# Optimization experiments

Hardware: AMD Instinct MI355X
Metric: run time of the kernel (lower is better)

Reference implementation:

```python
import jax, jax.numpy as jnp
import numpy as np
from jax import lax

NPOINT = 1024
NSAMPLE = 64
RADIUS = 0.2
EPS = 1e-5  # BatchNorm eps


def farthest_point_sample(xyz, npoint):
    # xyz: [B, N, 3] -> idx [B, npoint]; deterministic init at point 0
    B, N, _ = xyz.shape

    def step(carry, _):
        dist, farthest = carry
        centroid = jnp.take_along_axis(xyz, farthest[:, None, None], axis=1)  # [B,1,3]
        d = jnp.sum((xyz - centroid) ** 2, axis=-1)  # [B,N]
        dist = jnp.minimum(dist, d)
        new_far = jnp.argmax(dist, axis=-1).astype(jnp.int32)
        return (dist, new_far), farthest

    init = (jnp.full((B, N), 1e10, xyz.dtype), jnp.zeros((B,), jnp.int32))
    _, idxs = lax.scan(step, init, None, length=npoint)
    return jnp.transpose(idxs)  # [B, npoint]


def square_distance(src, dst):
    # src [B,S,3], dst [B,N,3] -> [B,S,N]
    d = -2.0 * jnp.einsum('bsc,bnc->bsn', src, dst)
    d += jnp.sum(src ** 2, -1)[:, :, None]
    d += jnp.sum(dst ** 2, -1)[:, None, :]
    return d


def query_ball_point(radius, nsample, xyz, new_xyz):
    B, N, _ = xyz.shape
    sqr = square_distance(new_xyz, xyz)  # [B,S,N]
    gi = jnp.where(sqr > radius ** 2, N, jnp.arange(N, dtype=jnp.int32))
    gi = jnp.sort(gi, axis=-1)[:, :, :nsample]  # [B,S,K]
    first = gi[:, :, :1]
    gi = jnp.where(gi == N, first, gi)
    return gi


def mlp_bn_relu(x, W, g, b):
    # x [B,S,K,Cin], W [Cin,Cout]; 1x1 conv + training-mode BN + ReLU
    y = jnp.einsum('bskc,co->bsko', x, W)
    m = jnp.mean(y, axis=(0, 1, 2))
    v = jnp.var(y, axis=(0, 1, 2))
    y = (y - m) * lax.rsqrt(v + EPS) * g + b
    return jax.nn.relu(y)


def setup_inputs() -> dict:
    key = jax.random.key(0)
    ks = jax.random.split(key, 8)
    B, N, C = 8, 4096, 128
    xyz = jax.random.uniform(ks[0], (B, N, 3), dtype=jnp.float32)
    features = jax.random.normal(ks[1], (B, C, N), dtype=jnp.float32)
    c_in = C + 3  # use_xyz
    W1 = jax.random.normal(ks[2], (c_in, 128), dtype=jnp.float32) * 0.05
    W2 = jax.random.normal(ks[3], (128, 128), dtype=jnp.float32) * 0.05
    W3 = jax.random.normal(ks[4], (128, 256), dtype=jnp.float32) * 0.05
    return {
        'xyz': xyz, 'features': features,
        'W1': W1, 'g1': jnp.ones((128,)), 'b1': jnp.zeros((128,)),
        'W2': W2, 'g2': jnp.ones((128,)), 'b2': jnp.zeros((128,)),
        'W3': W3, 'g3': jnp.ones((256,)), 'b3': jnp.zeros((256,)),
    }


def reference(xyz, features, W1, g1, b1, W2, g2, b2, W3, g3, b3):
    fps_idx = farthest_point_sample(xyz, NPOINT)              # [B,S]
    new_xyz = jnp.take_along_axis(xyz, fps_idx[:, :, None], axis=1)  # [B,S,3]
    gi = query_ball_point(RADIUS, NSAMPLE, xyz, new_xyz)      # [B,S,K]
    gather = jax.vmap(lambda p, i: p[i])                      # per-batch gather
    grouped_xyz = gather(xyz, gi) - new_xyz[:, :, None, :]    # [B,S,K,3]
    grouped_feat = gather(jnp.transpose(features, (0, 2, 1)), gi)  # [B,S,K,C]
    x = jnp.concatenate([grouped_xyz, grouped_feat], axis=-1)  # [B,S,K,3+C]
    x = mlp_bn_relu(x, W1, g1, b1)
    x = mlp_bn_relu(x, W2, g2, b2)
    x = mlp_bn_relu(x, W3, g3, b3)
    new_features = jnp.transpose(jnp.max(x, axis=2), (0, 2, 1))  # [B,256,S]
    return new_xyz, new_features
```

## Files before the change

kernel.cpp:

```cpp
#include <hip/hip_runtime.h>

#define B_  8
#define N_  4096
#define S_  1024
#define K_  64
#define CF_ 128
#define M_  (B_*S_*K_)

typedef __attribute__((ext_vector_type(8))) short bshort8;
typedef __attribute__((ext_vector_type(4))) float f32x4;
typedef __attribute__((ext_vector_type(4))) int   i32x4;
typedef __attribute__((ext_vector_type(2))) float f32x2;
typedef __attribute__((ext_vector_type(4))) unsigned short us4;

__device__ __forceinline__ unsigned short f2bf(float f){
  unsigned int u = __float_as_uint(f);
  u = u + 0x7FFFu + ((u >> 16) & 1u);
  return (unsigned short)(u >> 16);
}
__device__ __forceinline__ float bf2f(unsigned short h){
  return __uint_as_float(((unsigned int)h) << 16);
}

__device__ __forceinline__ void fused_stats(float* __restrict__ slots,
                                            const float* __restrict__ g,
                                            const float* __restrict__ beta,
                                            float* __restrict__ ssOut,
                                            int C, int* __restrict__ ctr,
                                            int nblocks, int t){
  __shared__ int lastFlag;
  __syncthreads();
  if (t == 0) lastFlag = (atomicAdd(ctr, 1) == nblocks - 1);
  __syncthreads();
  if (!lastFlag) return;
  if (t < C){
    const float inv_cnt = 1.0f/524288.0f;
    float s = 0.f, s2 = 0.f;
    for (int k = 0; k < 64; ++k){
      s  += atomicAdd(&slots[(k*C + t)*2 + 0], 0.0f);
      s2 += atomicAdd(&slots[(k*C + t)*2 + 1], 0.0f);
    }
    float m  = s * inv_cnt;
    float v  = fmaxf(s2 * inv_cnt - m*m, 0.f);
    float sc = rsqrtf(v + 1e-5f) * g[t];
    ssOut[t]     = sc;
    ssOut[C + t] = beta[t] - m*sc;
  }
}

__global__ __launch_bounds__(256) void prep_kernel(const float* __restrict__ f,
                                                   const float* __restrict__ W1,
                                                   const float* __restrict__ W2,
                                                   const float* __restrict__ W3,
                                                   unsigned short* __restrict__ ft,
                                                   unsigned short* __restrict__ Wt1,
                                                   unsigned short* __restrict__ Wt2,
                                                   unsigned short* __restrict__ Wt3){
  __shared__ float tile[32][33];
  const int blk = blockIdx.x;
  if (blk < 4096){
    int nt = blk & 127, ct = (blk>>7)&3, b = blk>>9;
    int tx = threadIdx.x & 31, ty = threadIdx.x >> 5;
#pragma unroll
    for (int r=0; r<32; r+=8)
      tile[ty+r][tx] = f[((size_t)(b*128 + ct*32 + ty + r))*4096 + nt*32 + tx];
    __syncthreads();
#pragma unroll
    for (int r=0; r<32; r+=8){
      int n = nt*32 + ty + r, cc = ct*32 + tx;
      ft[((size_t)b*4096 + n)*128 + cc] = f2bf(tile[tx][ty+r]);
    }
  } else {
    int t = (blk-4096)*256 + threadIdx.x;
    int stride = 64*256;
    for (int idx=t; idx<128*160; idx+=stride){
      int n = idx/160, k = idx-(idx/160)*160;
      float v = 0.f;
      if (k < 128) v = W1[(k+3)*128 + n];
      else if (k < 131) v = W1[(k-128)*128 + n];
      Wt1[idx] = f2bf(v);
    }
    for (int idx=t; idx<128*128; idx+=stride){
      int n = idx>>7, k = idx&127;
      Wt2[idx] = f2bf(W2[k*128+n]);
    }
    for (int idx=t; idx<256*128; idx+=stride){
      int n = idx>>7, k = idx&127;
      Wt3[idx] = f2bf(W3[k*256+n]);
    }
  }
}

__global__ __launch_bounds__(256,2) void pgemm_kernel(const unsigned short* __restrict__ featT,
                                                      const unsigned short* __restrict__ Wt1,
                                                      float* __restrict__ P){
  __shared__ alignas(16) unsigned short At[128*40];
  __shared__ alignas(16) unsigned short Bt[128*40];
  const int t = threadIdx.x, blk = blockIdx.x;
  const size_t rowBase = (size_t)blk*128;
  const int lane = t&63, wave = t>>6;
  const int wm = wave>>1, wn = wave&1;
  const int lrow = lane&15, quad = lane>>4;
  f32x4 acc[4][4];
  const f32x4 z4 = {0.f,0.f,0.f,0.f};
#pragma unroll
  for (int i=0;i<4;++i)
#pragma unroll
    for (int j=0;j<4;++j) acc[i][j]=z4;
  for (int ch=0; ch<4; ++ch){
    __syncthreads();
#pragma unroll
    for (int half=0; half<2; ++half){
      int sl = t + half*256; int r = sl>>2, p = sl&3;
      *(bshort8*)&At[r*40+p*8] = *(const bshort8*)(featT + (rowBase + r)*CF_ + ch*32 + p*8);
      *(bshort8*)&Bt[r*40+p*8] = *(const bshort8*)(Wt1 + r*160 + ch*32 + p*8);
    }
    __syncthreads();
    bshort8 af[4], bfr[4];
#pragma unroll
    for (int mt=0; mt<4; ++mt) af[mt]  = *(const bshort8*)&At[(wm*64+mt*16+lrow)*40 + quad*8];
#pragma unroll
    for (int nt=0; nt<4; ++nt) bfr[nt] = *(const bshort8*)&Bt[(wn*64+nt*16+lrow)*40 + quad*8];
#pragma unroll
    for (int mt=0; mt<4; ++mt)
#pragma unroll
      for (int nt=0; nt<4; ++nt)
        acc[mt][nt] = __builtin_amdgcn_mfma_f32_16x16x32_bf16(af[mt], bfr[nt], acc[mt][nt], 0,0,0);
  }
#pragma unroll
  for (int mt=0; mt<4; ++mt)
#pragma unroll
    for (int nt=0; nt<4; ++nt)
#pragma unroll
      for (int r=0; r<4; ++r){
        int row = wm*64 + mt*16 + quad*4 + r;
        int col = wn*64 + nt*16 + lrow;
        P[(rowBase + row)*128 + col] = acc[mt][nt][r];
      }
}

#define DPP_PAIR_STEP(CTRL)                                                     \
  {                                                                             \
    int _vi = __builtin_amdgcn_update_dpp(__float_as_int(best), __float_as_int(best), (CTRL), 0xF, 0xF, false); \
    int _ii = __builtin_amdgcn_update_dpp(bidx, bidx, (CTRL), 0xF, 0xF, false); \
    float _ov = __int_as_float(_vi);                                            \
    bool _tk = (_ov > best) || (_ov == best && _ii < bidx);                     \
    best = _tk ? _ov : best;                                                    \
    bidx = _tk ? _ii : bidx;                                                    \
  }

__global__ __launch_bounds__(256) void fps_kernel(const float* __restrict__ xyz,
                                                  float* __restrict__ nx_out,
                                                  float* __restrict__ nx_ws){
#pragma clang fp contract(off)
  __shared__ float sx[N_], sy[N_], sz[N_];
  __shared__ int   sidx[S_];
  __shared__ alignas(16) float redv[2][4];
  __shared__ alignas(16) int   redi[2][4];
  const int b = blockIdx.x, t = threadIdx.x;
  const int lane = t & 63, w = t >> 6;
  const float* xb = xyz + (size_t)b*N_*3;
  f32x2 px[8], py[8], pz[8], dist[8];
#pragma unroll
  for (int j=0;j<8;++j){
    int i0 = (2*j)*256 + t, i1 = (2*j+1)*256 + t;
    float x0=xb[i0*3+0], y0=xb[i0*3+1], z0=xb[i0*3+2];
    float x1=xb[i1*3+0], y1=xb[i1*3+1], z1=xb[i1*3+2];
    px[j] = (f32x2){x0,x1}; py[j] = (f32x2){y0,y1}; pz[j] = (f32x2){z0,z1};
    dist[j] = (f32x2){1e10f,1e10f};
    sx[i0]=x0; sy[i0]=y0; sz[i0]=z0;
    sx[i1]=x1; sy[i1]=y1; sz[i1]=z1;
  }
  __syncthreads();
  int farthest = 0;
  for (int it=0; it<S_; ++it){
    if (t==0) sidx[it] = farthest;
    float cx = sx[farthest], cy = sy[farthest], cz = sz[farthest];
    f32x2 cx2 = (f32x2){cx,cx}, cy2 = (f32x2){cy,cy}, cz2 = (f32x2){cz,cz};
    float best = -1.0f; int bidx = 0;
#pragma unroll
    for (int j=0;j<8;++j){
      f32x2 dx = px[j] - cx2;
      f32x2 dy = py[j] - cy2;
      f32x2 dz = pz[j] - cz2;
      f32x2 d  = (dx*dx + dy*dy) + dz*dz;
      f32x2 nd;
      nd.x = fminf(dist[j].x, d.x);
      nd.y = fminf(dist[j].y, d.y);
      dist[j] = nd;
      bool tk0 = nd.x > best;
      best = tk0 ? nd.x : best;
      bidx = tk0 ? ((2*j)*256 + t) : bidx;
      bool tk1 = nd.y > best;
      best = tk1 ? nd.y : best;
      bidx = tk1 ? ((2*j+1)*256 + t) : bidx;
    }
    DPP_PAIR_STEP(0xB1);
    DPP_PAIR_STEP(0x4E);
    DPP_PAIR_STEP(0x124);
    DPP_PAIR_STEP(0x128);
    DPP_PAIR_STEP(0x142);
    DPP_PAIR_STEP(0x143);
    const int buf = it & 1;
    if (lane == 63){ redv[buf][w] = best; redi[buf][w] = bidx; }
    __syncthreads();
    f32x4 vv = *(const f32x4*)&redv[buf][0];
    i32x4 iv = *(const i32x4*)&redi[buf][0];
    float v01 = vv[0]; int i01 = iv[0];
    { bool tk = (vv[1] > v01) || (vv[1] == v01 && iv[1] < i01); v01 = tk?vv[1]:v01; i01 = tk?iv[1]:i01; }
    float v23 = vv[2]; int i23 = iv[2];
    { bool tk = (vv[3] > v23) || (vv[3] == v23 && iv[3] < i23); v23 = tk?vv[3]:v23; i23 = tk?iv[3]:i23; }
    { bool tk = (v23 > v01) || (v23 == v01 && i23 < i01); v01 = tk?v23:v01; i01 = tk?i23:i01; }
    farthest = i01;
  }
  __syncthreads();
  for (int i=t; i<S_; i+=256){
    int id = sidx[i];
    size_t base = (size_t)(b*S_+i)*3;
    float vx=sx[id], vy=sy[id], vz=sz[id];
    nx_out[base+0]=vx; nx_out[base+1]=vy; nx_out[base+2]=vz;
    nx_ws[base+0]=vx;  nx_ws[base+1]=vy;  nx_ws[base+2]=vz;
  }
}

__global__ __launch_bounds__(256) void qbp_y1_kernel(const float* __restrict__ xyz,
                                                     const float* __restrict__ nx,
                                                     const float* __restrict__ P,
                                                     const float* __restrict__ W1,
                                                     int* __restrict__ gi,
                                                     float* __restrict__ slots,
                                                     const float* __restrict__ g1,
                                                     const float* __restrict__ b1,
                                                     float* __restrict__ ss1,
                                                     int* __restrict__ ctr){
  __shared__ int giW[4][64];
  __shared__ alignas(16) float dxL[4][64][4];
  __shared__ float sLDS[128], s2LDS[128];
  const int t = threadIdx.x;
  const int lane = t & 63, w = t >> 6;
  if (t < 128){ sLDS[t]=0.f; s2LDS[t]=0.f; }
  __syncthreads();
  const int wid = blockIdx.x*4 + w;
  const int b = wid >> 10, s = wid & 1023;
  const float* xb = xyz + (size_t)b*N_*3;
  {
    const double R2 = 0.2*0.2;
    const float* c  = nx + (size_t)(b*S_+s)*3;
    double cx=(double)c[0], cy=(double)c[1], cz=(double)c[2];
    double cc = cx*cx + cy*cy + cz*cz;
    int* g = gi + (size_t)(b*S_+s)*K_;
    int count = 0, first = -1;
    for (int ch=0; ch<64 && count<K_; ++ch){
      int i = ch*64 + lane;
      double x = (double)xb[i*3+0], y = (double)xb[i*3+1], z = (double)xb[i*3+2];
      double e  = cx*x + cy*y + cz*z;
      double pp = x*x + y*y + z*z;
      double d  = -2.0*e + cc + pp;
      bool keep = !(d > R2);
      unsigned long long bal = __ballot(keep);
      int pos = count + __builtin_popcountll(bal & ((1ull<<lane)-1ull));
      if (keep && pos < K_){ g[pos] = i; giW[w][pos] = i; }
      if (first < 0 && bal) first = ch*64 + (int)__builtin_ctzll(bal);
      count += __builtin_popcountll(bal);
    }
    if (count < K_){
      int p = count + lane;
      if (p < K_){ g[p] = first; giW[w][p] = first; }
    }
    int i = giW[w][lane];
    const float* pp = xyz + ((size_t)b*N_ + i)*3;
    const float* qq = nx  + (size_t)(b*S_ + s)*3;
    dxL[w][lane][0] = __fsub_rn(pp[0],qq[0]);
    dxL[w][lane][1] = __fsub_rn(pp[1],qq[1]);
    dxL[w][lane][2] = __fsub_rn(pp[2],qq[2]);
  }
  {
    const int cq = lane*2;
    f32x2 w0 = *(const f32x2*)(W1 + cq);
    f32x2 w1v = *(const f32x2*)(W1 + 128 + cq);
    f32x2 w2 = *(const f32x2*)(W1 + 256 + cq);
    f32x2 sA = {0,0}, s2A = {0,0};
#pragma unroll 4
    for (int r=0; r<64; ++r){
      int pi = giW[w][r];
      f32x2 p = *(const f32x2*)(P + ((size_t)b*N_ + pi)*128 + cq);
      float dx = dxL[w][r][0], dy = dxL[w][r][1], dz = dxL[w][r][2];
      f32x2 y;
#pragma unroll
      for (int e=0;e<2;++e)
        y[e] = fmaf(dz, w2[e], fmaf(dy, w1v[e], fmaf(dx, w0[e], p[e])));
      sA.x += y.x; sA.y += y.y;
      s2A.x = fmaf(y.x,y.x,s2A.x); s2A.y = fmaf(y.y,y.y,s2A.y);
    }
    atomicAdd(&sLDS[cq],    sA.x);  atomicAdd(&sLDS[cq+1],  sA.y);
    atomicAdd(&s2LDS[cq],   s2A.x); atomicAdd(&s2LDS[cq+1], s2A.y);
  }
  __syncthreads();
  if (t < 128){
    int slot = blockIdx.x & 63;
    atomicAdd(&slots[(slot*128+t)*2+0], sLDS[t]);
    atomicAdd(&slots[(slot*128+t)*2+1], s2LDS[t]);
  }
  fused_stats(slots, g1, b1, ss1, 128, ctr, 2048, t);
}

template<int PHASE, bool STOREY2>
__global__ __launch_bounds__(256,2) void mm_fused(
    const float* __restrict__ P,
    const float* __restrict__ W1,
    const unsigned short* __restrict__ Wt2,
    const unsigned short* __restrict__ Wt3,
    const int* __restrict__ gi,
    const float* __restrict__ xyz,
    const float* __restrict__ nxyz,
    const float* __restrict__ ss1,
    const float* __restrict__ ss2,
    float* __restrict__ slots,
    float* __restrict__ minv,
    float* __restrict__ maxv,
    unsigned short* __restrict__ y2out,
    const float* __restrict__ gg,
    const float* __restrict__ bb,
    float* __restrict__ ssOut,
    int* __restrict__ ctr)
{
  __shared__ alignas(16) unsigned short Bt[2][128*40];
  __shared__ alignas(16) unsigned short Y[128*136];
  __shared__ int giL[128];
  __shared__ alignas(16) float dxL[128][4];
  __shared__ alignas(16) float w0L[128], w1L[128], w2L[128];

  const int t = threadIdx.x;
  const int mblk = blockIdx.x;
  const int b = mblk >> 9;
  const int lane = t&63, wave = t>>6;
  const int wm = wave>>1, wn = wave&1;
  const int lrow = lane&15, quad = lane>>4;
  const int slot = mblk & 63;

  if (t<128){
    int i = gi[(size_t)mblk*128 + t];
    giL[t] = i;
    int s = ((mblk*128 + t) >> 6) & 1023;
    const float* pp = xyz  + ((size_t)b*N_ + i)*3;
    const float* qq = nxyz + (size_t)(b*S_ + s)*3;
    dxL[t][0] = __fsub_rn(pp[0],qq[0]);
    dxL[t][1] = __fsub_rn(pp[1],qq[1]);
    dxL[t][2] = __fsub_rn(pp[2],qq[2]);
    w0L[t] = W1[t]; w1L[t] = W1[128+t]; w2L[t] = W1[256+t];
  }
  __syncthreads();

  {
    const int rgrp = t>>5, cq = (t&31)*4;
    f32x4 w0 = *(const f32x4*)&w0L[cq];
    f32x4 w1 = *(const f32x4*)&w1L[cq];
    f32x4 w2 = *(const f32x4*)&w2L[cq];
    f32x4 a1v = *(const f32x4*)(ss1 + cq);
    f32x4 b1v = *(const f32x4*)(ss1 + 128 + cq);
#pragma unroll
    for (int g=0; g<16; ++g){
      int r = g*8 + rgrp;
      int pi = giL[r];
      f32x4 p = *(const f32x4*)(P + ((size_t)b*N_ + pi)*128 + cq);
      float dx = dxL[r][0], dy = dxL[r][1], dz = dxL[r][2];
      f32x4 y;
#pragma unroll
      for (int e=0;e<4;++e)
        y[e] = fmaf(dz, w2[e], fmaf(dy, w1[e], fmaf(dx, w0[e], p[e])));
      us4 zz;
#pragma unroll
      for (int e=0;e<4;++e)
        zz[e] = f2bf(fmaxf(fmaf(y[e], a1v[e], b1v[e]), 0.f));
      *(us4*)&Y[r*136 + cq] = zz;
    }
  }

  f32x4 acc[4][4];
  const f32x4 z4 = {0.f,0.f,0.f,0.f};
#pragma unroll
  for (int i=0;i<4;++i)
#pragma unroll
    for (int j=0;j<4;++j) acc[i][j]=z4;

  {
    bshort8 bV[2];
#pragma unroll
    for (int half=0; half<2; ++half){
      int sl = t + half*256; int r = sl>>2, p = sl&3;
      bV[half] = *(const bshort8*)(Wt2 + r*128 + p*8);
    }
#pragma unroll
    for (int half=0; half<2; ++half){
      int sl = t + half*256; int r = sl>>2, p = sl&3;
      *(bshort8*)&Bt[1][r*40+p*8] = bV[half];
    }
    for (int ch=0; ch<4; ++ch){
      const int cur = (ch & 1) ^ 1;
      __syncthreads();
      bshort8 af[4], bfr[4];
#pragma unroll
      for (int mt=0; mt<4; ++mt) af[mt]  = *(const bshort8*)&Y[(wm*64+mt*16+lrow)*136 + ch*32 + quad*8];
#pragma unroll
      for (int nt=0; nt<4; ++nt) bfr[nt] = *(const bshort8*)&Bt[cur][(wn*64+nt*16+lrow)*40 + quad*8];
      if (ch < 3){
#pragma unroll
        for (int half=0; half<2; ++half){
          int sl = t + half*256; int r = sl>>2, p = sl&3;
          bV[half] = *(const bshort8*)(Wt2 + r*128 + (ch+1)*32 + p*8);
        }
      }
#pragma unroll
      for (int mt=0; mt<4; ++mt)
#pragma unroll
        for (int nt=0; nt<4; ++nt)
          acc[mt][nt] = __builtin_amdgcn_mfma_f32_16x16x32_bf16(af[mt], bfr[nt], acc[mt][nt], 0,0,0);
      if (ch < 3){
        const int nxt = cur ^ 1;
#pragma unroll
        for (int half=0; half<2; ++half){
          int sl = t + half*256; int r = sl>>2, p = sl&3;
          *(bshort8*)&Bt[nxt][r*40+p*8] = bV[half];
        }
      }
    }
  }

  if constexpr (PHASE==2){
#pragma unroll
    for (int nt=0; nt<4; ++nt){
      float s=0.f, s2=0.f;
#pragma unroll
      for (int mt=0; mt<4; ++mt)
#pragma unroll
        for (int r=0; r<4; ++r){ float v=acc[mt][nt][r]; s+=v; s2=fmaf(v,v,s2); }
      s  += __shfl_xor(s,16,64);  s  += __shfl_xor(s,32,64);
      s2 += __shfl_xor(s2,16,64); s2 += __shfl_xor(s2,32,64);
      if (lane<16){
        int c = wn*64+nt*16+lane;
        atomicAdd(&slots[(slot*128+c)*2+0], s);
        atomicAdd(&slots[(slot*128+c)*2+1], s2);
      }
    }
    if constexpr (STOREY2){
      __syncthreads();
#pragma unroll
      for (int nt=0; nt<4; ++nt){
        int c = wn*64+nt*16+lrow;
#pragma unroll
        for (int mt=0; mt<4; ++mt)
#pragma unroll
          for (int r=0; r<4; ++r){
            int row = wm*64+mt*16+quad*4+r;
            Y[row*136 + c] = f2bf(acc[mt][nt][r]);
          }
      }
      __syncthreads();
      for (int idx=t; idx<128*16; idx+=256){
        int r = idx>>4, p = idx&15;
        bshort8 v = *(const bshort8*)&Y[r*136 + p*8];
        *(bshort8*)(y2out + ((size_t)mblk*128 + r)*128 + p*8) = v;
      }
    }
    fused_stats(slots, gg, bb, ssOut, 128, ctr, 4096, t);
    return;
  }

  if constexpr (PHASE==3){
    __syncthreads();
#pragma unroll
    for (int nt=0; nt<4; ++nt){
      int c = wn*64+nt*16+lrow;
      float sc = ss2[c], sh = ss2[128+c];
#pragma unroll
      for (int mt=0; mt<4; ++mt)
#pragma unroll
        for (int r=0; r<4; ++r){
          int row = wm*64+mt*16+quad*4+r;
          Y[row*136 + c] = f2bf(fmaxf(fmaf(acc[mt][nt][r], sc, sh), 0.f));
        }
    }

    for (int h=0; h<2; ++h){
#pragma unroll
      for (int i=0;i<4;++i)
#pragma unroll
        for (int j=0;j<4;++j) acc[i][j]=z4;
      bshort8 bV[2];
#pragma unroll
      for (int half=0; half<2; ++half){
        int sl = t + half*256; int r = sl>>2, p = sl&3;
        bV[half] = *(const bshort8*)(Wt3 + ((size_t)(h*128+r))*128 + p*8);
      }
#pragma unroll
      for (int half=0; half<2; ++half){
        int sl = t + half*256; int r = sl>>2, p = sl&3;
        *(bshort8*)&Bt[1][r*40+p*8] = bV[half];
      }
      for (int ch=0; ch<4; ++ch){
        const int cur = (ch & 1) ^ 1;
        __syncthreads();
        bshort8 af[4], bfr[4];
#pragma unroll
        for (int mt=0; mt<4; ++mt) af[mt]  = *(const bshort8*)&Y[(wm*64+mt*16+lrow)*136 + ch*32 + quad*8];
#pragma unroll
        for (int nt=0; nt<4; ++nt) bfr[nt] = *(const bshort8*)&Bt[cur][(wn*64+nt*16+lrow)*40 + quad*8];
        if (ch < 3){
#pragma unroll
          for (int half=0; half<2; ++half){
            int sl = t + half*256; int r = sl>>2, p = sl&3;
            bV[half] = *(const bshort8*)(Wt3 + ((size_t)(h*128+r))*128 + (ch+1)*32 + p*8);
          }
        }
#pragma unroll
        for (int mt=0; mt<4; ++mt)
#pragma unroll
          for (int nt=0; nt<4; ++nt)
            acc[mt][nt] = __builtin_amdgcn_mfma_f32_16x16x32_bf16(af[mt], bfr[nt], acc[mt][nt], 0,0,0);
        if (ch < 3){
          const int nxt = cur ^ 1;
#pragma unroll
          for (int half=0; half<2; ++half){
            int sl = t + half*256; int r = sl>>2, p = sl&3;
            *(bshort8*)&Bt[nxt][r*40+p*8] = bV[half];
          }
        }
      }
#pragma unroll
      for (int nt=0; nt<4; ++nt){
        float s=0.f, s2=0.f, mx=-3.0e38f, mn=3.0e38f;
#pragma unroll
        for (int mt=0; mt<4; ++mt)
#pragma unroll
          for (int r=0; r<4; ++r){
            float v=acc[mt][nt][r];
            s+=v; s2=fmaf(v,v,s2);
            mx=fmaxf(mx,v); mn=fminf(mn,v);
          }
        s  += __shfl_xor(s,16,64);  s  += __shfl_xor(s,32,64);
        s2 += __shfl_xor(s2,16,64); s2 += __shfl_xor(s2,32,64);
        mx = fmaxf(mx, __shfl_xor(mx,16,64)); mx = fmaxf(mx, __shfl_xor(mx,32,64));
        mn = fminf(mn, __shfl_xor(mn,16,64)); mn = fminf(mn, __shfl_xor(mn,32,64));
        if (lane<16){
          int c = h*128 + wn*64+nt*16+lane;
          atomicAdd(&slots[(slot*256+c)*2+0], s);
          atomicAdd(&slots[(slot*256+c)*2+1], s2);
          size_t sidx = (size_t)mblk*2 + wm;
          maxv[sidx*256 + c] = mx;
          minv[sidx*256 + c] = mn;
        }
      }
    }
    fused_stats(slots, gg, bb, ssOut, 256, ctr, 4096, t);
  }
}

__global__ __launch_bounds__(256,2) void mm3_kernel(
    const unsigned short* __restrict__ y2,
    const unsigned short* __restrict__ Wt3,
    const float* __restrict__ ss2,
    float* __restrict__ slots,
    float* __restrict__ minv,
    float* __restrict__ maxv,
    const float* __restrict__ g3,
    const float* __restrict__ b3,
    float* __restrict__ ss3,
    int* __restrict__ ctr)
{
  __shared__ alignas(16) unsigned short Bt[2][128*40];
  __shared__ alignas(16) unsigned short Y[128*136];
  const int t = threadIdx.x;
  const int mblk = blockIdx.x;
  const int lane = t&63, wave = t>>6;
  const int wm = wave>>1, wn = wave&1;
  const int lrow = lane&15, quad = lane>>4;
  const int slot = mblk & 63;

  {
    const int rgrp = t>>5, cq = (t&31)*4;
    f32x4 a2 = *(const f32x4*)(ss2 + cq);
    f32x4 b2 = *(const f32x4*)(ss2 + 128 + cq);
#pragma unroll
    for (int g=0; g<16; ++g){
      int r = g*8 + rgrp;
      us4 yv = *(const us4*)(y2 + ((size_t)mblk*128 + r)*128 + cq);
      us4 zz;
#pragma unroll
      for (int e=0;e<4;++e)
        zz[e] = f2bf(fmaxf(fmaf(bf2f(yv[e]), a2[e], b2[e]), 0.f));
      *(us4*)&Y[r*136 + cq] = zz;
    }
  }

  f32x4 acc[4][4];
  const f32x4 z4 = {0.f,0.f,0.f,0.f};
  for (int h=0; h<2; ++h){
#pragma unroll
    for (int i=0;i<4;++i)
#pragma unroll
      for (int j=0;j<4;++j) acc[i][j]=z4;
    bshort8 bV[2];
#pragma unroll
    for (int half=0; half<2; ++half){
      int sl = t + half*256; int r = sl>>2, p = sl&3;
      bV[half] = *(const bshort8*)(Wt3 + ((size_t)(h*128+r))*128 + p*8);
    }
#pragma unroll
    for (int half=0; half<2; ++half){
      int sl = t + half*256; int r = sl>>2, p = sl&3;
      *(bshort8*)&Bt[1][r*40+p*8] = bV[half];
    }
    for (int ch=0; ch<4; ++ch){
      const int cur = (ch & 1) ^ 1;
      __syncthreads();
      bshort8 af[4], bfr[4];
#pragma unroll
      for (int mt=0; mt<4; ++mt) af[mt]  = *(const bshort8*)&Y[(wm*64+mt*16+lrow)*136 + ch*32 + quad*8];
#pragma unroll
      for (int nt=0; nt<4; ++nt) bfr[nt] = *(const bshort8*)&Bt[cur][(wn*64+nt*16+lrow)*40 + quad*8];
      if (ch < 3){
#pragma unroll
        for (int half=0; half<2; ++half){
          int sl = t + half*256; int r = sl>>2, p = sl&3;
          bV[half] = *(const bshort8*)(Wt3 + ((size_t)(h*128+r))*128 + (ch+1)*32 + p*8);
        }
      }
#pragma unroll
      for (int mt=0; mt<4; ++mt)
#pragma unroll
        for (int nt=0; nt<4; ++nt)
          acc[mt][nt] = __builtin_amdgcn_mfma_f32_16x16x32_bf16(af[mt], bfr[nt], acc[mt][nt], 0,0,0);
      if (ch < 3){
        const int nxt = cur ^ 1;
#pragma unroll
        for (int half=0; half<2; ++half){
          int sl = t + half*256; int r = sl>>2, p = sl&3;
          *(bshort8*)&Bt[nxt][r*40+p*8] = bV[half];
        }
      }
    }
#pragma unroll
    for (int nt=0; nt<4; ++nt){
      float s=0.f, s2=0.f, mx=-3.0e38f, mn=3.0e38f;
#pragma unroll
      for (int mt=0; mt<4; ++mt)
#pragma unroll
        for (int r=0; r<4; ++r){
          float v=acc[mt][nt][r];
          s+=v; s2=fmaf(v,v,s2);
          mx=fmaxf(mx,v); mn=fminf(mn,v);
        }
      s  += __shfl_xor(s,16,64);  s  += __shfl_xor(s,32,64);
      s2 += __shfl_xor(s2,16,64); s2 += __shfl_xor(s2,32,64);
      mx = fmaxf(mx, __shfl_xor(mx,16,64)); mx = fmaxf(mx, __shfl_xor(mx,32,64));
      mn = fminf(mn, __shfl_xor(mn,16,64)); mn = fminf(mn, __shfl_xor(mn,32,64));
      if (lane<16){
        int c = h*128 + wn*64+nt*16+lane;
        atomicAdd(&slots[(slot*256+c)*2+0], s);
        atomicAdd(&slots[(slot*256+c)*2+1], s2);
        size_t sidx = (size_t)mblk*2 + wm;
        maxv[sidx*256 + c] = mx;
        minv[sidx*256 + c] = mn;
      }
    }
    if (h==0) __syncthreads();
  }
  fused_stats(slots, g3, b3, ss3, 256, ctr, 4096, t);
}

__global__ __launch_bounds__(256) void final_kernel(const float* __restrict__ minv,
                                                    const float* __restrict__ maxv,
                                                    const float* __restrict__ ss3,
                                                    float* __restrict__ out){
  __shared__ float tile[64][65];
  const int t = threadIdx.x;
  const int cb = blockIdx.x;
  const int sb = blockIdx.y;
  const int b  = blockIdx.z;
  const int w = t>>6, l = t&63;
  {
    int c = cb*64 + l;
    float sc = ss3[c], sh = ss3[256+c];
#pragma unroll
    for (int k=0;k<16;++k){
      int sl = k*4 + w;
      size_t mi = ((size_t)(b*1024 + sb*64 + sl))*256 + c;
      float v = (sc >= 0.f) ? maxv[mi] : minv[mi];
      tile[sl][l] = fmaxf(fmaf(v, sc, sh), 0.f);
    }
  }
  __syncthreads();
#pragma unroll
  for (int k=0;k<16;++k){
    int cl = k*4 + w;
    out[((size_t)(b*256 + cb*64 + cl))*1024 + sb*64 + l] = tile[l][cl];
  }
}

extern "C" void kernel_launch(void* const* d_in, const int* in_sizes, int n_in,
                              void* d_out, int out_size, void* d_ws, size_t ws_size,
                              hipStream_t stream){
  const float* xyz      = (const float*)d_in[0];
  const float* features = (const float*)d_in[1];
  const float* W1 = (const float*)d_in[2];
  const float* g1 = (const float*)d_in[3];
  const float* b1 = (const float*)d_in[4];
  const float* W2 = (const float*)d_in[5];
  const float* g2 = (const float*)d_in[6];
  const float* b2 = (const float*)d_in[7];
  const float* W3 = (const float*)d_in[8];
  const float* g3 = (const float*)d_in[9];
  const float* b3 = (const float*)d_in[10];
  float* out = (float*)d_out;

  char* ws = (char*)d_ws;
  size_t off = 0;
  auto alloc = [&](size_t bytes)->char*{
    char* p = ws + off;
    off = (off + bytes + 255) & ~(size_t)255;
    return p;
  };
  float* slots1 = (float*)alloc((size_t)64*128*2*4);
  float* slots2 = (float*)alloc((size_t)64*128*2*4);
  float* slots3 = (float*)alloc((size_t)64*256*2*4);
  int*   ctrs   = (int*)  alloc(256);
  float* ss1    = (float*)alloc(256*4);
  float* ss2    = (float*)alloc(256*4);
  float* ss3    = (float*)alloc(512*4);
  float* nxyz   = (float*)alloc((size_t)24576*4);
  int*   gi     = (int*)  alloc((size_t)M_*4);
  unsigned short* featT = (unsigned short*)alloc((size_t)B_*N_*CF_*2);
  unsigned short* Wt1   = (unsigned short*)alloc((size_t)128*160*2);
  unsigned short* Wt2   = (unsigned short*)alloc((size_t)128*128*2);
  unsigned short* Wt3   = (unsigned short*)alloc((size_t)256*128*2);
  float* minv = (float*)alloc((size_t)B_*S_*256*4);
  float* maxv = (float*)alloc((size_t)B_*S_*256*4);
  float* P    = (float*)alloc((size_t)B_*N_*128*4);
  size_t base_end = off;
  unsigned short* y2 = (unsigned short*)alloc((size_t)M_*128*2);
  const bool bigws = (off <= ws_size);
  (void)base_end;

  hipMemsetAsync(slots1, 0, (size_t)(64*128*2 + 64*128*2 + 64*256*2)*4 + 256, stream);

  prep_kernel<<<4160, 256, 0, stream>>>(features, W1, W2, W3, featT, Wt1, Wt2, Wt3);
  pgemm_kernel<<<256, 256, 0, stream>>>(featT, Wt1, P);
  fps_kernel<<<8, 256, 0, stream>>>(xyz, out, nxyz);
  qbp_y1_kernel<<<2048, 256, 0, stream>>>(xyz, nxyz, P, W1, gi, slots1, g1, b1, ss1, ctrs+0);

  if (bigws){
    mm_fused<2,true><<<4096, 256, 0, stream>>>(P, W1, Wt2, Wt3, gi, xyz, nxyz,
                                               ss1, nullptr, slots2, nullptr, nullptr, y2,
                                               g2, b2, ss2, ctrs+1);
    mm3_kernel<<<4096, 256, 0, stream>>>(y2, Wt3, ss2, slots3, minv, maxv,
                                         g3, b3, ss3, ctrs+2);
  } else {
    mm_fused<2,false><<<4096, 256, 0, stream>>>(P, W1, Wt2, Wt3, gi, xyz, nxyz,
                                                ss1, nullptr, slots2, nullptr, nullptr, nullptr,
                                                g2, b2, ss2, ctrs+1);
    mm_fused<3,false><<<4096, 256, 0, stream>>>(P, W1, Wt2, Wt3, gi, xyz, nxyz,
                                                ss1, ss2, slots3, minv, maxv, nullptr,
                                                g3, b3, ss3, ctrs+2);
  }
  final_kernel<<<dim3(4,16,8), 256, 0, stream>>>(minv, maxv, ss3, out + 24576);
}
```

Measured before the change: 1.128 ms.

## Replace last-block fused BN stats with separate stats kernels; tree-reduce FPS argmax

Removes the atomic-counter last-block pattern that finished the batch-norm statistics at the end of each big kernel, and launches a small single-block stats_kernel between stages instead. This drops the extra block-wide syncs and global atomic per block, at the cost of three extra tiny launches. Separately, the FPS per-thread argmax over 16 points becomes a tree of pairwise selects rather than a serial chain, which shortens the dependency chain inside the 1024-iteration serial loop. Tie-breaking in the tree prefers the lower slot on equal values, matching the serial version.

```diff
diff --git a/kernel.cpp b/kernel.cpp
--- a/kernel.cpp
+++ b/kernel.cpp
@@ -20,32 +20,6 @@
 }
 __device__ __forceinline__ float bf2f(unsigned short h){
   return __uint_as_float(((unsigned int)h) << 16);
-}
-
-__device__ __forceinline__ void fused_stats(float* __restrict__ slots,
-                                            const float* __restrict__ g,
-                                            const float* __restrict__ beta,
-                                            float* __restrict__ ssOut,
-                                            int C, int* __restrict__ ctr,
-                                            int nblocks, int t){
-  __shared__ int lastFlag;
-  __syncthreads();
-  if (t == 0) lastFlag = (atomicAdd(ctr, 1) == nblocks - 1);
-  __syncthreads();
-  if (!lastFlag) return;
-  if (t < C){
-    const float inv_cnt = 1.0f/524288.0f;
-    float s = 0.f, s2 = 0.f;
-    for (int k = 0; k < 64; ++k){
-      s  += atomicAdd(&slots[(k*C + t)*2 + 0], 0.0f);
-      s2 += atomicAdd(&slots[(k*C + t)*2 + 1], 0.0f);
-    }
-    float m  = s * inv_cnt;
-    float v  = fmaxf(s2 * inv_cnt - m*m, 0.f);
-    float sc = rsqrtf(v + 1e-5f) * g[t];
-    ssOut[t]     = sc;
-    ssOut[C + t] = beta[t] - m*sc;
-  }
 }
 
 __global__ __launch_bounds__(256) void prep_kernel(const float* __restrict__ f,
@@ -177,7 +151,6 @@
     if (t==0) sidx[it] = farthest;
     float cx = sx[farthest], cy = sy[farthest], cz = sz[farthest];
     f32x2 cx2 = (f32x2){cx,cx}, cy2 = (f32x2){cy,cy}, cz2 = (f32x2){cz,cz};
-    float best = -1.0f; int bidx = 0;
 #pragma unroll
     for (int j=0;j<8;++j){
       f32x2 dx = px[j] - cx2;
@@ -188,13 +161,35 @@
       nd.x = fminf(dist[j].x, d.x);
       nd.y = fminf(dist[j].y, d.y);
       dist[j] = nd;
-      bool tk0 = nd.x > best;
-      best = tk0 ? nd.x : best;
-      bidx = tk0 ? ((2*j)*256 + t) : bidx;
-      bool tk1 = nd.y > best;
-      best = tk1 ? nd.y : best;
-      bidx = tk1 ? ((2*j+1)*256 + t) : bidx;
-    }
+    }
+    float v0[8]; int s0[8];
+#pragma unroll
+    for (int j=0;j<8;++j){
+      bool tk = dist[j].y > dist[j].x;
+      v0[j] = tk ? dist[j].y : dist[j].x;
+      s0[j] = tk ? (2*j+1) : (2*j);
+    }
+    float v1[4]; int s1[4];
+#pragma unroll
+    for (int j=0;j<4;++j){
+      bool tk = v0[2*j+1] > v0[2*j];
+      v1[j] = tk ? v0[2*j+1] : v0[2*j];
+      s1[j] = tk ? s0[2*j+1] : s0[2*j];
+    }
+    float v2[2]; int s2[2];
+#pragma unroll
+    for (int j=0;j<2;++j){
+      bool tk = v1[2*j+1] > v1[2*j];
+      v2[j] = tk ? v1[2*j+1] : v1[2*j];
+      s2[j] = tk ? s1[2*j+1] : s1[2*j];
+    }
+    float best; int slot;
+    {
+      bool tk = v2[1] > v2[0];
+      best = tk ? v2[1] : v2[0];
+      slot = tk ? s2[1] : s2[0];
+    }
+    int bidx = (slot << 8) + t;
     DPP_PAIR_STEP(0xB1);
     DPP_PAIR_STEP(0x4E);
     DPP_PAIR_STEP(0x124);
@@ -228,11 +223,7 @@
                                                      const float* __restrict__ P,
                                                      const float* __restrict__ W1,
                                                      int* __restrict__ gi,
-                                                     float* __restrict__ slots,
-                                                     const float* __restrict__ g1,
-                                                     const float* __restrict__ b1,
-                                                     float* __restrict__ ss1,
-                                                     int* __restrict__ ctr){
+                                                     float* __restrict__ slots){
   __shared__ int giW[4][64];
   __shared__ alignas(16) float dxL[4][64][4];
   __shared__ float sLDS[128], s2LDS[128];
@@ -301,7 +292,6 @@
     atomicAdd(&slots[(slot*128+t)*2+0], sLDS[t]);
     atomicAdd(&slots[(slot*128+t)*2+1], s2LDS[t]);
   }
-  fused_stats(slots, g1, b1, ss1, 128, ctr, 2048, t);
 }
 
 template<int PHASE, bool STOREY2>
@@ -318,11 +308,7 @@
     float* __restrict__ slots,
     float* __restrict__ minv,
     float* __restrict__ maxv,
-    unsigned short* __restrict__ y2out,
-    const float* __restrict__ gg,
-    const float* __restrict__ bb,
-    float* __restrict__ ssOut,
-    int* __restrict__ ctr)
+    unsigned short* __restrict__ y2out)
 {
   __shared__ alignas(16) unsigned short Bt[2][128*40];
   __shared__ alignas(16) unsigned short Y[128*136];
@@ -462,7 +448,6 @@
         *(bshort8*)(y2out + ((size_t)mblk*128 + r)*128 + p*8) = v;
       }
     }
-    fused_stats(slots, gg, bb, ssOut, 128, ctr, 4096, t);
     return;
   }
 
@@ -551,7 +536,6 @@
         }
       }
     }
-    fused_stats(slots, gg, bb, ssOut, 256, ctr, 4096, t);
   }
 }
 
@@ -561,11 +545,7 @@
     const float* __restrict__ ss2,
     float* __restrict__ slots,
     float* __restrict__ minv,
-    float* __restrict__ maxv,
-    const float* __restrict__ g3,
-    const float* __restrict__ b3,
-    float* __restrict__ ss3,
-    int* __restrict__ ctr)
+    float* __restrict__ maxv)
 {
   __shared__ alignas(16) unsigned short Bt[2][128*40];
   __shared__ alignas(16) unsigned short Y[128*136];
@@ -665,7 +645,23 @@
     }
     if (h==0) __syncthreads();
   }
-  fused_stats(slots, g3, b3, ss3, 256, ctr, 4096, t);
+}
+
+__global__ void stats_kernel(const float* __restrict__ slots, const float* __restrict__ g,
+                             const float* __restrict__ beta, float* __restrict__ ssOut,
+                             int C, float inv_cnt){
+  int c = threadIdx.x;
+  if (c >= C) return;
+  float s=0.f, s2=0.f;
+  for (int k=0;k<64;++k){
+    s  += slots[(k*C + c)*2 + 0];
+    s2 += slots[(k*C + c)*2 + 1];
+  }
+  float m = s * inv_cnt;
+  float v = fmaxf(s2 * inv_cnt - m*m, 0.f);
+  float sc = rsqrtf(v + 1e-5f) * g[c];
+  ssOut[c] = sc;
+  ssOut[C + c] = beta[c] - m*sc;
 }
 
 __global__ __launch_bounds__(256) void final_kernel(const float* __restrict__ minv,
@@ -723,7 +719,6 @@
   float* slots1 = (float*)alloc((size_t)64*128*2*4);
   float* slots2 = (float*)alloc((size_t)64*128*2*4);
   float* slots3 = (float*)alloc((size_t)64*256*2*4);
-  int*   ctrs   = (int*)  alloc(256);
   float* ss1    = (float*)alloc(256*4);
   float* ss2    = (float*)alloc(256*4);
   float* ss3    = (float*)alloc(512*4);
@@ -741,26 +736,27 @@
   const bool bigws = (off <= ws_size);
   (void)base_end;
 
-  hipMemsetAsync(slots1, 0, (size_t)(64*128*2 + 64*128*2 + 64*256*2)*4 + 256, stream);
+  hipMemsetAsync(slots1, 0, (size_t)(64*128*2 + 64*128*2 + 64*256*2)*4, stream);
 
   prep_kernel<<<4160, 256, 0, stream>>>(features, W1, W2, W3, featT, Wt1, Wt2, Wt3);
   pgemm_kernel<<<256, 256, 0, stream>>>(featT, Wt1, P);
   fps_kernel<<<8, 256, 0, stream>>>(xyz, out, nxyz);
-  qbp_y1_kernel<<<2048, 256, 0, stream>>>(xyz, nxyz, P, W1, gi, slots1, g1, b1, ss1, ctrs+0);
-
+  qbp_y1_kernel<<<2048, 256, 0, stream>>>(xyz, nxyz, P, W1, gi, slots1);
+
+  const float inv_cnt = 1.0f / (float)M_;
+  stats_kernel<<<1, 128, 0, stream>>>(slots1, g1, b1, ss1, 128, inv_cnt);
   if (bigws){
     mm_fused<2,true><<<4096, 256, 0, stream>>>(P, W1, Wt2, Wt3, gi, xyz, nxyz,
-                                               ss1, nullptr, slots2, nullptr, nullptr, y2,
-                                               g2, b2, ss2, ctrs+1);
-    mm3_kernel<<<4096, 256, 0, stream>>>(y2, Wt3, ss2, slots3, minv, maxv,
-                                         g3, b3, ss3, ctrs+2);
+                                               ss1, nullptr, slots2, nullptr, nullptr, y2);
+    stats_kernel<<<1, 128, 0, stream>>>(slots2, g2, b2, ss2, 128, inv_cnt);
+    mm3_kernel<<<4096, 256, 0, stream>>>(y2, Wt3, ss2, slots3, minv, maxv);
   } else {
     mm_fused<2,false><<<4096, 256, 0, stream>>>(P, W1, Wt2, Wt3, gi, xyz, nxyz,
-                                                ss1, nullptr, slots2, nullptr, nullptr, nullptr,
-                                                g2, b2, ss2, ctrs+1);
+                                                ss1, nullptr, slots2, nullptr, nullptr, nullptr);
+    stats_kernel<<<1, 128, 0, stream>>>(slots2, g2, b2, ss2, 128, inv_cnt);
     mm_fused<3,false><<<4096, 256, 0, stream>>>(P, W1, Wt2, Wt3, gi, xyz, nxyz,
-                                                ss1, ss2, slots3, minv, maxv, nullptr,
-                                                g3, b3, ss3, ctrs+2);
-  }
+                                                ss1, ss2, slots3, minv, maxv, nullptr);
+  }
+  stats_kernel<<<1, 256, 0, stream>>>(slots3, g3, b3, ss3, 256, inv_cnt);
   final_kernel<<<dim3(4,16,8), 256, 0, stream>>>(minv, maxv, ss3, out + 24576);
 }
```

Measured after the change: 1.262 ms. 11.8% more time.
